# Kernel optimization log

Hardware: AMD Instinct MI355X
Metric: run time of the kernel (lower is better)

## Reference

```python
import jax, jax.numpy as jnp
import numpy as np

D_MODEL = 1024
DIM_K = 1024
DIM_V = 1024
N_HEADS = 16
B, SX, SY = 4, 1024, 1024
NORM_FACT = float(1.0 / np.sqrt(D_MODEL))  # note: 1/sqrt(d_model), not head dim


def setup_inputs() -> dict:
    key = jax.random.key(0)
    ks = jax.random.split(key, 10)
    s = 0.02
    return {
        "x": jax.random.normal(ks[0], (B, SX, D_MODEL), jnp.float32),
        "y": jax.random.normal(ks[1], (B, SY, D_MODEL), jnp.float32),
        "Wq": jax.random.normal(ks[2], (DIM_K, D_MODEL), jnp.float32) * s,
        "bq": jax.random.normal(ks[3], (DIM_K,), jnp.float32) * s,
        "Wk": jax.random.normal(ks[4], (DIM_K, D_MODEL), jnp.float32) * s,
        "bk": jax.random.normal(ks[5], (DIM_K,), jnp.float32) * s,
        "Wv": jax.random.normal(ks[6], (DIM_V, D_MODEL), jnp.float32) * s,
        "bv": jax.random.normal(ks[7], (DIM_V,), jnp.float32) * s,
        "Wo": jax.random.normal(ks[8], (D_MODEL, DIM_V), jnp.float32) * s,
        "bo": jax.random.normal(ks[9], (D_MODEL,), jnp.float32) * s,
        "requires_mask": 1,
    }


def reference(x, y, Wq, bq, Wk, bk, Wv, bv, Wo, bo, requires_mask):
    b, sx, _ = x.shape
    sy = y.shape[1]
    dk_h = DIM_K // N_HEADS
    dv_h = DIM_V // N_HEADS
    # torch: q(x).reshape(-1, B, S, dk_h) -> raw row-major reshape puts heads first
    Q = (x @ Wq.T + bq).reshape(N_HEADS, b, sx, dk_h)
    K = (y @ Wk.T + bk).reshape(N_HEADS, b, sy, dk_h)
    V = (y @ Wv.T + bv).reshape(N_HEADS, b, sy, dv_h)

    score = jnp.einsum('hbsd,hbtd->hbst', Q, K) * NORM_FACT  # [H,B,Sx,Sy]
    # branch 1: softmax over query axis (-2), then L1-normalize rows
    attn = jax.nn.softmax(score, axis=-2)
    l1 = jnp.maximum(jnp.sum(jnp.abs(attn), axis=-1, keepdims=True), 1e-12)
    attn = attn / l1
    # branch 2: mean-threshold mask then row softmax
    score1 = score
    if requires_mask:
        thre = jnp.mean(score, axis=-1, keepdims=True)
        score1 = jnp.where(score - thre > 0, score, -jnp.inf)
    attn1 = jax.nn.softmax(score1, axis=-1)

    # torch: matmul(...).reshape(B, Sx, -1) -> raw reshape of [H,B,Sx,dv_h]
    out = jnp.einsum('hbst,hbtd->hbsd', attn, V).reshape(b, sx, -1)
    out1 = jnp.einsum('hbst,hbtd->hbsd', attn1, V).reshape(b, sx, -1)
    out = 0.5 * (out + out1)
    return out @ Wo.T + bo
```

## Files before the change

kernel.cpp:

```cpp
#include <hip/hip_runtime.h>
#include <hip/hip_bf16.h>
#include <stdint.h>

typedef float f32x4 __attribute__((ext_vector_type(4)));
typedef short bf16x8 __attribute__((ext_vector_type(8)));
typedef _Float16 f16x8 __attribute__((ext_vector_type(8)));

#define DEV static __device__ __forceinline__

DEV float bf2f(short u) {
  union { float f; unsigned i; } v;
  v.i = ((unsigned)(unsigned short)u) << 16;
  return v.f;
}
DEV short f2bf(float f) {
  union { float f; unsigned i; } v;
  v.f = f;
  unsigned lsb = (v.i >> 16) & 1u;
  v.i += 0x7fffu + lsb;
  return (short)(v.i >> 16);
}
DEV short f2h(float f) {
  union { _Float16 h; short s; } u;
  u.h = (_Float16)f;
  return u.s;
}

DEV void glds16(const void* g, void* l) {
  __builtin_amdgcn_global_load_lds(
      (const __attribute__((address_space(1))) void*)g,
      (__attribute__((address_space(3))) void*)l, 16, 0, 0);
}

__global__ __launch_bounds__(256) void k_convert(
    const float* __restrict__ x, const float* __restrict__ y,
    const float* __restrict__ wq, const float* __restrict__ wk,
    const float* __restrict__ wv, const float* __restrict__ wo,
    short* __restrict__ x16, short* __restrict__ y16,
    short* __restrict__ wq16, short* __restrict__ wk16,
    short* __restrict__ wv16, short* __restrict__ wohi) {
  const float* src; short* dst; int n, half;
  switch (blockIdx.y) {
    case 0: src = x;  dst = x16;  n = 4194304; half = 1; break;
    case 1: src = y;  dst = y16;  n = 4194304; half = 1; break;
    case 2: src = wq; dst = wq16; n = 1048576; half = 1; break;
    case 3: src = wk; dst = wk16; n = 1048576; half = 1; break;
    case 4: src = wv; dst = wv16; n = 1048576; half = 1; break;
    default: src = wo; dst = wohi; n = 1048576; half = 0; break;
  }
  int i4 = blockIdx.x * 256 + threadIdx.x;
  if (i4 * 4 >= n) return;
  float4 v = ((const float4*)src)[i4];
  short4 h;
  float* pv = (float*)&v;
  short* ph = (short*)&h;
#pragma unroll
  for (int e = 0; e < 4; ++e) ph[e] = half ? f2h(pv[e]) : f2bf(pv[e]);
  ((short4*)dst)[i4] = h;
}

DEV void gemm_block_map(int wg, long& bRow, long& bCol) {
  int rlow = wg & 7, c = (wg >> 3) & 7, rhigh = wg >> 6;
  bRow = (long)(rhigh * 8 + rlow) * 128;
  bCol = (long)c * 128;
}

__global__ __launch_bounds__(512) void k_gemm_out(
    const short* __restrict__ A, const short* __restrict__ B,
    const float* __restrict__ bias, float* __restrict__ C, int M, int N, int K) {
  __shared__ __align__(16) short As[2][128 * 64];
  __shared__ __align__(16) short Bs[2][128 * 64];
  const int tid = threadIdx.x, lane = tid & 63;
  const int w = tid >> 6, wr = w >> 1, wc = w & 1;
  const int lo = lane & 15, hi4 = lane >> 4;
  long bRow, bCol;
  gemm_block_map(blockIdx.x, bRow, bCol);
  f32x4 acc[2][4] = {};
  const int nks = K >> 6;
  auto stage = [&](int buf, int ks) {
#pragma unroll
    for (int i = 0; i < 2; ++i) {
      int c = i * 512 + tid;
      int r = c >> 3;
      int wi = ((c & 7) * 16) ^ ((r & 7) << 4);
      glds16((const char*)A + (bRow + r) * (long)(K * 2) + ks * 128 + wi, (char*)As[buf] + c * 16);
      glds16((const char*)B + (bCol + r) * (long)(K * 2) + ks * 128 + wi, (char*)Bs[buf] + c * 16);
    }
  };
  stage(0, 0);
  __syncthreads();
  int p = 0;
  for (int ks = 0; ks < nks; ++ks) {
    if (ks + 1 < nks) stage(p ^ 1, ks + 1);
#pragma unroll
    for (int kk = 0; kk < 2; ++kk) {
      bf16x8 af[2], bfr[4];
#pragma unroll
      for (int m = 0; m < 2; ++m) {
        int r = wr * 32 + m * 16 + lo;
        af[m] = *(const bf16x8*)((const char*)As[p] + r * 128 + ((kk * 64 + hi4 * 16) ^ ((r & 7) << 4)));
      }
#pragma unroll
      for (int n = 0; n < 4; ++n) {
        int r = wc * 64 + n * 16 + lo;
        bfr[n] = *(const bf16x8*)((const char*)Bs[p] + r * 128 + ((kk * 64 + hi4 * 16) ^ ((r & 7) << 4)));
      }
#pragma unroll
      for (int m = 0; m < 2; ++m)
#pragma unroll
        for (int n = 0; n < 4; ++n)
          acc[m][n] = __builtin_amdgcn_mfma_f32_16x16x32_bf16(af[m], bfr[n], acc[m][n], 0, 0, 0);
    }
    __syncthreads();
    p ^= 1;
  }
#pragma unroll
  for (int n = 0; n < 4; ++n) {
    long col = bCol + wc * 64 + n * 16 + lo;
    float bv = bias[col];
#pragma unroll
    for (int m = 0; m < 2; ++m) {
      long row0 = bRow + wr * 32 + m * 16 + hi4 * 4;
#pragma unroll
      for (int j = 0; j < 4; ++j)
        C[(row0 + j) * N + col] = acc[m][n][j] + bv;
    }
  }
}

template <int OUT_MODE>
__global__ __launch_bounds__(512) void k_gemm_f16(
    const short* __restrict__ A, const short* __restrict__ B,
    const float* __restrict__ bias, short* __restrict__ C, int M, int N, int K) {
  __shared__ __align__(16) short As[2][128 * 64];
  __shared__ __align__(16) short Bs[2][128 * 64];
  const int tid = threadIdx.x, lane = tid & 63;
  const int w = tid >> 6, wr = w >> 1, wc = w & 1;
  const int lo = lane & 15, hi4 = lane >> 4;
  long bRow, bCol;
  gemm_block_map(blockIdx.x, bRow, bCol);
  f32x4 acc[2][4] = {};
  const int nks = K >> 6;
  auto stage = [&](int buf, int ks) {
#pragma unroll
    for (int i = 0; i < 2; ++i) {
      int c = i * 512 + tid;
      int r = c >> 3;
      int wi = ((c & 7) * 16) ^ ((r & 7) << 4);
      glds16((const char*)A + (bRow + r) * (long)(K * 2) + ks * 128 + wi, (char*)As[buf] + c * 16);
      glds16((const char*)B + (bCol + r) * (long)(K * 2) + ks * 128 + wi, (char*)Bs[buf] + c * 16);
    }
  };
  stage(0, 0);
  __syncthreads();
  int p = 0;
  for (int ks = 0; ks < nks; ++ks) {
    if (ks + 1 < nks) stage(p ^ 1, ks + 1);
#pragma unroll
    for (int kk = 0; kk < 2; ++kk) {
      f16x8 af[2], bfr[4];
#pragma unroll
      for (int m = 0; m < 2; ++m) {
        int r = wr * 32 + m * 16 + lo;
        af[m] = *(const f16x8*)((const char*)As[p] + r * 128 + ((kk * 64 + hi4 * 16) ^ ((r & 7) << 4)));
      }
#pragma unroll
      for (int n = 0; n < 4; ++n) {
        int r = wc * 64 + n * 16 + lo;
        bfr[n] = *(const f16x8*)((const char*)Bs[p] + r * 128 + ((kk * 64 + hi4 * 16) ^ ((r & 7) << 4)));
      }
#pragma unroll
      for (int m = 0; m < 2; ++m)
#pragma unroll
        for (int n = 0; n < 4; ++n)
          acc[m][n] = __builtin_amdgcn_mfma_f32_16x16x32_f16(af[m], bfr[n], acc[m][n], 0, 0, 0);
    }
    __syncthreads();
    p ^= 1;
  }
#pragma unroll
  for (int n = 0; n < 4; ++n) {
    long col = bCol + wc * 64 + n * 16 + lo;
    float bv = bias[col];
#pragma unroll
    for (int m = 0; m < 2; ++m)
#pragma unroll
      for (int j = 0; j < 4; ++j) {
        long row = bRow + wr * 32 + m * 16 + hi4 * 4 + j;
        float v = acc[m][n][j] + bv;
        C[row * N + col] = (OUT_MODE == 2) ? f2h(v) : f2bf(v);
      }
  }
}

__global__ __launch_bounds__(256) void k_transpose_scale(
    const short* __restrict__ Vb, const float* __restrict__ rL,
    short* __restrict__ Vt, short* __restrict__ rlbf) {
  __shared__ __align__(16) short T[64][264];
  int g = blockIdx.y, t0 = blockIdx.x * 256;
  int tid = threadIdx.x;
  const short* src = Vb + (long)g * 65536;
  const float* rlp = rL + g * 1024 + t0;
#pragma unroll
  for (int i = 0; i < 8; ++i) {
    int c = i * 256 + tid;
    int t = c >> 3, dc = (c & 7) * 8;
    bf16x8 v = *(const bf16x8*)(src + (long)(t0 + t) * 64 + dc);
    float rv = rlp[t];
#pragma unroll
    for (int e = 0; e < 8; ++e) T[dc + e][t] = f2bf(bf2f(v[e]) * rv);
  }
  rlbf[g * 1024 + t0 + tid] = f2bf(rlp[tid]);
  __syncthreads();
  short* dst = Vt + (long)g * 65536;
#pragma unroll
  for (int i = 0; i < 8; ++i) {
    int c = i * 256 + tid;
    int d = c >> 5, tc = (c & 31) * 8;
    bf16x8 v = *(const bf16x8*)(&T[d][tc]);
    *(bf16x8*)(dst + (long)d * 1024 + t0 + tc) = v;
  }
}

__global__ __launch_bounds__(256) void k_mu(
    const short* __restrict__ K16, const short* __restrict__ Q16,
    float* __restrict__ Thr) {
  __shared__ float tmp[32][64];
  __shared__ float ksum[64];
  const int g = blockIdx.x >> 2, q = blockIdx.x & 3;
  const int tid = threadIdx.x;
  const int d8 = tid & 7, tq = tid >> 3;
  const short* kp = K16 + (long)g * 65536;
  float acc[8] = {};
  for (int t = tq; t < 1024; t += 32) {
    f16x8 a = *(const f16x8*)(kp + t * 64 + d8 * 8);
#pragma unroll
    for (int e = 0; e < 8; ++e) acc[e] += (float)a[e];
  }
#pragma unroll
  for (int e = 0; e < 8; ++e) tmp[tq][d8 * 8 + e] = acc[e];
  __syncthreads();
  if (tid < 64) {
    float s = 0.f;
#pragma unroll
    for (int qq = 0; qq < 32; ++qq) s += tmp[qq][tid];
    ksum[tid] = s;
  }
  __syncthreads();
  const float c = 0.03125f / 1024.f;
  const int s = q * 256 + tid;
  const short* qp = Q16 + (long)g * 65536 + s * 64;
  float dot = 0.f;
#pragma unroll
  for (int d0 = 0; d0 < 64; d0 += 8) {
    f16x8 a = *(const f16x8*)(qp + d0);
#pragma unroll
    for (int e = 0; e < 8; ++e) dot += (float)a[e] * ksum[d0 + e];
  }
  Thr[g * 1024 + s] = dot * c;
}

__global__ __launch_bounds__(256) void k_passA(
    const short* __restrict__ Q16, const short* __restrict__ K16,
    float* __restrict__ rL) {
  __shared__ __align__(16) short Ks[64 * 64];
  __shared__ __align__(16) short Qs[2][64 * 64];
  const int wg = blockIdx.x;
  const int g = (wg & 7) | ((wg >> 7) << 3);
  const int tb = (wg >> 3) & 15;
  const int tid = threadIdx.x, lane = tid & 63;
  const int w = tid >> 6;
  const int lo = lane & 15, hi4 = lane >> 4;
  const long gbase = (long)g * 131072;
  const float CEXP = 0.045136860026163146f;

  auto stageQ = [&](int buf, int sb) {
#pragma unroll
    for (int i = 0; i < 2; ++i) {
      int c = i * 256 + tid;
      int r = c >> 3;
      int wi = ((c & 7) * 16) ^ ((r & 7) << 4);
      glds16((const char*)Q16 + gbase + (long)(sb * 64 + r) * 128 + wi, (char*)Qs[buf] + c * 16);
    }
  };
#pragma unroll
  for (int i = 0; i < 2; ++i) {
    int c = i * 256 + tid;
    int r = c >> 3;
    int wi = ((c & 7) * 16) ^ ((r & 7) << 4);
    glds16((const char*)K16 + gbase + (long)(tb * 64 + r) * 128 + wi, (char*)Ks + c * 16);
  }
  stageQ(0, 0);
  __syncthreads();
  f16x8 kf[2];
#pragma unroll
  for (int kk = 0; kk < 2; ++kk) {
    int r = w * 16 + lo;
    kf[kk] = *(const f16x8*)((const char*)Ks + r * 128 + ((kk * 64 + hi4 * 16) ^ ((r & 7) << 4)));
  }
  float Lacc[4] = {};
  int p = 0;
  for (int sb = 0; sb < 16; ++sb) {
    if (sb < 15) stageQ(p ^ 1, sb + 1);
    f32x4 s[4] = {};
#pragma unroll
    for (int kk = 0; kk < 2; ++kk) {
#pragma unroll
      for (int n = 0; n < 4; ++n) {
        int r = n * 16 + lo;
        f16x8 qf = *(const f16x8*)((const char*)Qs[p] + r * 128 +
                                   ((kk * 64 + hi4 * 16) ^ ((r & 7) << 4)));
        __builtin_amdgcn_s_setprio(1);
        s[n] = __builtin_amdgcn_mfma_f32_16x16x32_f16(kf[kk], qf, s[n], 0, 0, 0);
        __builtin_amdgcn_s_setprio(0);
      }
    }
#pragma unroll
    for (int n = 0; n < 4; ++n)
#pragma unroll
      for (int j = 0; j < 4; ++j)
        Lacc[j] += __builtin_amdgcn_exp2f(s[n][j] * CEXP);
    __syncthreads();
    p ^= 1;
  }
#pragma unroll
  for (int j = 0; j < 4; ++j) {
    float v = Lacc[j];
    v += __shfl_xor(v, 1);
    v += __shfl_xor(v, 2);
    v += __shfl_xor(v, 4);
    v += __shfl_xor(v, 8);
    if (lo == 0) rL[g * 1024 + tb * 64 + w * 16 + hi4 * 4 + j] = 1.0f / v;
  }
}

__global__ __launch_bounds__(256, 4) void k_passB(
    const short* __restrict__ Q16, const short* __restrict__ K16,
    const short* __restrict__ Vt, const short* __restrict__ rlbf,
    const float* __restrict__ Thr, short* __restrict__ Pre,
    const int* __restrict__ rmask) {
  __shared__ __align__(16) short Ks[2][64 * 64];
  __shared__ __align__(16) short Vs[2][64 * 64];
  __shared__ __align__(16) short Ps[64 * 64];
  const int wg = blockIdx.x;
  const int g = (wg & 7) | ((wg >> 7) << 3);
  const int rb = (wg >> 3) & 15;
  const int tid = threadIdx.x, lane = tid & 63;
  const int w = tid >> 6;
  const int lo = lane & 15, hi4 = lane >> 4;
  const long gbase = (long)g * 131072;
  const bool use_mask = (*rmask != 0);
  const int srow = w * 16 + lo;

  auto stage = [&](int buf, int tb2) {
#pragma unroll
    for (int i = 0; i < 2; ++i) {
      int c = i * 256 + tid;
      int r = c >> 3;
      int wi = ((c & 7) * 16) ^ ((r & 7) << 4);
      glds16((const char*)K16 + gbase + (long)(tb2 * 64 + r) * 128 + wi, (char*)Ks[buf] + c * 16);
      glds16((const char*)Vt + gbase + (long)r * 2048 + tb2 * 128 + wi, (char*)Vs[buf] + c * 16);
    }
  };

  f16x8 qf[2];
  {
    const char* qr = (const char*)Q16 + gbase + (long)(rb * 64 + srow) * 128;
#pragma unroll
    for (int kk = 0; kk < 2; ++kk)
      qf[kk] = *(const f16x8*)(qr + kk * 64 + hi4 * 16);
  }
  const float thre32 = use_mask ? Thr[g * 1024 + rb * 64 + srow] * 32.0f : -3.4e38f;
  const float CEXP = 0.045136860026163146f;
  f32x4 o1[4] = {}, o2[4] = {};
  f32x4 o1R = {}, o2Z = {};

  stage(0, 0);
  __syncthreads();
  int p = 0;
  for (int tb = 0; tb < 16; ++tb) {
    if (tb < 15) stage(p ^ 1, tb + 1);
    f32x4 s[4] = {};
#pragma unroll
    for (int kk = 0; kk < 2; ++kk) {
#pragma unroll
      for (int n = 0; n < 4; ++n) {
        int r = n * 16 + lo;
        f16x8 kf = *(const f16x8*)((const char*)Ks[p] + r * 128 +
                                   ((kk * 64 + hi4 * 16) ^ ((r & 7) << 4)));
        __builtin_amdgcn_s_setprio(1);
        s[n] = __builtin_amdgcn_mfma_f32_16x16x32_f16(kf, qf[kk], s[n], 0, 0, 0);
        __builtin_amdgcn_s_setprio(0);
      }
    }
    unsigned p2w0[4], p2w1[4];
#pragma unroll
    for (int n = 0; n < 4; ++n) {
      float ev[4], p2v[4];
#pragma unroll
      for (int j = 0; j < 4; ++j) {
        float sraw = s[n][j];
        float e = __builtin_amdgcn_exp2f(sraw * CEXP);
        ev[j] = e;
        p2v[j] = (sraw > thre32) ? e : 0.f;
      }
      unsigned u10, u11, u20, u21;
      asm("v_cvt_pk_bf16_f32 %0, %1, %2" : "=v"(u10) : "v"(ev[0]), "v"(ev[1]));
      asm("v_cvt_pk_bf16_f32 %0, %1, %2" : "=v"(u11) : "v"(ev[2]), "v"(ev[3]));
      asm("v_cvt_pk_bf16_f32 %0, %1, %2" : "=v"(u20) : "v"(p2v[0]), "v"(p2v[1]));
      asm("v_cvt_pk_bf16_f32 %0, %1, %2" : "=v"(u21) : "v"(p2v[2]), "v"(p2v[3]));
      p2w0[n] = u20;
      p2w1[n] = u21;
      int colb = n * 32 + hi4 * 8;
      int boff = srow * 128 + (colb ^ ((srow & 7) << 4));
      uint2 w1; w1.x = u10; w1.y = u11;
      *(uint2*)((char*)Ps + boff) = w1;
    }
    bf16x8 vbreg[2][4], rlfr[2];
#pragma unroll
    for (int kk = 0; kk < 2; ++kk) {
      int poff = srow * 128 + ((kk * 64 + hi4 * 16) ^ ((srow & 7) << 4));
      bf16x8 pa1 = *(const bf16x8*)((const char*)Ps + poff);
      rlfr[kk] = *(const bf16x8*)(rlbf + g * 1024 + tb * 64 + kk * 32 + hi4 * 8);
      __builtin_amdgcn_s_setprio(1);
      o1R = __builtin_amdgcn_mfma_f32_16x16x32_bf16(pa1, rlfr[kk], o1R, 0, 0, 0);
      __builtin_amdgcn_s_setprio(0);
#pragma unroll
      for (int n = 0; n < 4; ++n) {
        int d = n * 16 + lo;
        vbreg[kk][n] = *(const bf16x8*)((const char*)Vs[p] + d * 128 +
                                        ((kk * 64 + hi4 * 16) ^ ((d & 7) << 4)));
        __builtin_amdgcn_s_setprio(1);
        o1[n] = __builtin_amdgcn_mfma_f32_16x16x32_bf16(pa1, vbreg[kk][n], o1[n], 0, 0, 0);
        __builtin_amdgcn_s_setprio(0);
      }
    }
#pragma unroll
    for (int n = 0; n < 4; ++n) {
      int colb = n * 32 + hi4 * 8;
      int boff = srow * 128 + (colb ^ ((srow & 7) << 4));
      uint2 w2; w2.x = p2w0[n]; w2.y = p2w1[n];
      *(uint2*)((char*)Ps + boff) = w2;
    }
#pragma unroll
    for (int kk = 0; kk < 2; ++kk) {
      int poff = srow * 128 + ((kk * 64 + hi4 * 16) ^ ((srow & 7) << 4));
      bf16x8 pa2 = *(const bf16x8*)((const char*)Ps + poff);
      __builtin_amdgcn_s_setprio(1);
      o2Z = __builtin_amdgcn_mfma_f32_16x16x32_bf16(pa2, rlfr[kk], o2Z, 0, 0, 0);
#pragma unroll
      for (int n = 0; n < 4; ++n)
        o2[n] = __builtin_amdgcn_mfma_f32_16x16x32_bf16(pa2, vbreg[kk][n], o2[n], 0, 0, 0);
      __builtin_amdgcn_s_setprio(0);
    }
    __syncthreads();
    p ^= 1;
  }
#pragma unroll
  for (int j = 0; j < 4; ++j) {
    float rr = fmaxf(o1R[j], 1e-12f);
    float zz = fmaxf(o2Z[j], 1e-30f);
    float rinv = 0.5f / rr;
    float zinv = 0.5f / zz;
    int rl_ = w * 16 + hi4 * 4 + j;
#pragma unroll
    for (int n = 0; n < 4; ++n) {
      float val = o1[n][j] * rinv + o2[n][j] * zinv;
      Pre[(long)g * 65536 + (long)(rb * 64 + rl_) * 64 + n * 16 + lo] = f2bf(val);
    }
  }
}

extern "C" void kernel_launch(void* const* d_in, const int* in_sizes, int n_in,
                              void* d_out, int out_size, void* d_ws, size_t ws_size,
                              hipStream_t stream) {
  const float* x  = (const float*)d_in[0];
  const float* y  = (const float*)d_in[1];
  const float* Wq = (const float*)d_in[2];
  const float* bq = (const float*)d_in[3];
  const float* Wk = (const float*)d_in[4];
  const float* bk = (const float*)d_in[5];
  const float* Wv = (const float*)d_in[6];
  const float* bv = (const float*)d_in[7];
  const float* Wo = (const float*)d_in[8];
  const float* bo = (const float*)d_in[9];
  const int* rm   = (const int*)d_in[10];
  float* out = (float*)d_out;

  char* ws = (char*)d_ws;
  size_t off = 0;
  auto alloc = [&](size_t bytes) {
    char* p = ws + off;
    off += (bytes + 255) & ~(size_t)255;
    return p;
  };
  short* x16  = (short*)alloc(4194304 * 2);
  short* y16  = (short*)alloc(4194304 * 2);
  short* wq16 = (short*)alloc(1048576 * 2);
  short* wk16 = (short*)alloc(1048576 * 2);
  short* wv16 = (short*)alloc(1048576 * 2);
  short* wohi = (short*)alloc(1048576 * 2);
  short* Q16  = (short*)alloc(4194304 * 2);
  short* K16  = (short*)alloc(4194304 * 2);
  short* Vb   = (short*)alloc(4194304 * 2);
  short* VtB  = (short*)alloc(4194304 * 2);
  short* pre  = (short*)alloc(4194304 * 2);
  float* rLbuf = (float*)alloc(65536 * 4);
  short* rlbf  = (short*)alloc(65536 * 2);
  float* Thr   = (float*)alloc(65536 * 4);
  if (off > ws_size) return;

  k_convert<<<dim3(4096, 6), 256, 0, stream>>>(x, y, Wq, Wk, Wv, Wo,
                                               x16, y16, wq16, wk16, wv16, wohi);

  k_gemm_f16<2><<<256, 512, 0, stream>>>(x16, wq16, bq, Q16, 4096, 1024, 1024);
  k_gemm_f16<2><<<256, 512, 0, stream>>>(y16, wk16, bk, K16, 4096, 1024, 1024);
  k_gemm_f16<0><<<256, 512, 0, stream>>>(y16, wv16, bv, Vb, 4096, 1024, 1024);
  k_mu<<<256, 256, 0, stream>>>(K16, Q16, Thr);
  k_passA<<<1024, 256, 0, stream>>>(Q16, K16, rLbuf);
  k_transpose_scale<<<dim3(4, 64), 256, 0, stream>>>(Vb, rLbuf, VtB, rlbf);
  k_passB<<<1024, 256, 0, stream>>>(Q16, K16, VtB, rlbf, Thr, pre, rm);
  k_gemm_out<<<256, 512, 0, stream>>>(pre, wohi, bo, out, 4096, 1024, 1024);
}
```

Before: 161.2 us.

## Fuse V transpose-scale into passA and retile GEMMs to 128x64 blocks

Drops the separate transpose/scale kernel. Each passA block now loads its own 64-token V tile, scales it by the reciprocal column sums it just computed, transposes it through shared memory and writes Vt and the bf16 scales directly, which removes one launch and the fp32 rL round trip. All four GEMMs move from 512-thread 128x128 tiles to 256-thread 128x64 tiles with 512 blocks, giving more blocks per GPU and less shared memory per block at the cost of more A-tile reloads.

After: 156.0 us. 1.03x faster.

```diff
diff --git a/kernel.cpp b/kernel.cpp
--- a/kernel.cpp
+++ b/kernel.cpp
@@ -59,31 +59,37 @@
   ((short4*)dst)[i4] = h;
 }
 
-DEV void gemm_block_map(int wg, long& bRow, long& bCol) {
-  int rlow = wg & 7, c = (wg >> 3) & 7, rhigh = wg >> 6;
+DEV void gemm_block_map64(int wg, long& bRow, long& bCol) {
+  int rlow = wg & 7, c = (wg >> 3) & 15, rhigh = wg >> 7;
   bRow = (long)(rhigh * 8 + rlow) * 128;
-  bCol = (long)c * 128;
-}
-
-__global__ __launch_bounds__(512) void k_gemm_out(
+  bCol = (long)c * 64;
+}
+
+__global__ __launch_bounds__(256) void k_gemm_out(
     const short* __restrict__ A, const short* __restrict__ B,
     const float* __restrict__ bias, float* __restrict__ C, int M, int N, int K) {
   __shared__ __align__(16) short As[2][128 * 64];
-  __shared__ __align__(16) short Bs[2][128 * 64];
+  __shared__ __align__(16) short Bs[2][64 * 64];
   const int tid = threadIdx.x, lane = tid & 63;
-  const int w = tid >> 6, wr = w >> 1, wc = w & 1;
+  const int w = tid >> 6;
   const int lo = lane & 15, hi4 = lane >> 4;
   long bRow, bCol;
-  gemm_block_map(blockIdx.x, bRow, bCol);
+  gemm_block_map64(blockIdx.x, bRow, bCol);
   f32x4 acc[2][4] = {};
   const int nks = K >> 6;
   auto stage = [&](int buf, int ks) {
 #pragma unroll
-    for (int i = 0; i < 2; ++i) {
-      int c = i * 512 + tid;
+    for (int i = 0; i < 4; ++i) {
+      int c = i * 256 + tid;
       int r = c >> 3;
       int wi = ((c & 7) * 16) ^ ((r & 7) << 4);
       glds16((const char*)A + (bRow + r) * (long)(K * 2) + ks * 128 + wi, (char*)As[buf] + c * 16);
+    }
+#pragma unroll
+    for (int i = 0; i < 2; ++i) {
+      int c = i * 256 + tid;
+      int r = c >> 3;
+      int wi = ((c & 7) * 16) ^ ((r & 7) << 4);
       glds16((const char*)B + (bCol + r) * (long)(K * 2) + ks * 128 + wi, (char*)Bs[buf] + c * 16);
     }
   };
@@ -97,12 +103,12 @@
       bf16x8 af[2], bfr[4];
 #pragma unroll
       for (int m = 0; m < 2; ++m) {
-        int r = wr * 32 + m * 16 + lo;
+        int r = w * 32 + m * 16 + lo;
         af[m] = *(const bf16x8*)((const char*)As[p] + r * 128 + ((kk * 64 + hi4 * 16) ^ ((r & 7) << 4)));
       }
 #pragma unroll
       for (int n = 0; n < 4; ++n) {
-        int r = wc * 64 + n * 16 + lo;
+        int r = n * 16 + lo;
         bfr[n] = *(const bf16x8*)((const char*)Bs[p] + r * 128 + ((kk * 64 + hi4 * 16) ^ ((r & 7) << 4)));
       }
 #pragma unroll
@@ -116,11 +122,11 @@
   }
 #pragma unroll
   for (int n = 0; n < 4; ++n) {
-    long col = bCol + wc * 64 + n * 16 + lo;
+    long col = bCol + n * 16 + lo;
     float bv = bias[col];
 #pragma unroll
     for (int m = 0; m < 2; ++m) {
-      long row0 = bRow + wr * 32 + m * 16 + hi4 * 4;
+      long row0 = bRow + w * 32 + m * 16 + hi4 * 4;
 #pragma unroll
       for (int j = 0; j < 4; ++j)
         C[(row0 + j) * N + col] = acc[m][n][j] + bv;
@@ -129,25 +135,31 @@
 }
 
 template <int OUT_MODE>
-__global__ __launch_bounds__(512) void k_gemm_f16(
+__global__ __launch_bounds__(256) void k_gemm_f16(
     const short* __restrict__ A, const short* __restrict__ B,
     const float* __restrict__ bias, short* __restrict__ C, int M, int N, int K) {
   __shared__ __align__(16) short As[2][128 * 64];
-  __shared__ __align__(16) short Bs[2][128 * 64];
+  __shared__ __align__(16) short Bs[2][64 * 64];
   const int tid = threadIdx.x, lane = tid & 63;
-  const int w = tid >> 6, wr = w >> 1, wc = w & 1;
+  const int w = tid >> 6;
   const int lo = lane & 15, hi4 = lane >> 4;
   long bRow, bCol;
-  gemm_block_map(blockIdx.x, bRow, bCol);
+  gemm_block_map64(blockIdx.x, bRow, bCol);
   f32x4 acc[2][4] = {};
   const int nks = K >> 6;
   auto stage = [&](int buf, int ks) {
 #pragma unroll
-    for (int i = 0; i < 2; ++i) {
-      int c = i * 512 + tid;
+    for (int i = 0; i < 4; ++i) {
+      int c = i * 256 + tid;
       int r = c >> 3;
       int wi = ((c & 7) * 16) ^ ((r & 7) << 4);
       glds16((const char*)A + (bRow + r) * (long)(K * 2) + ks * 128 + wi, (char*)As[buf] + c * 16);
+    }
+#pragma unroll
+    for (int i = 0; i < 2; ++i) {
+      int c = i * 256 + tid;
+      int r = c >> 3;
+      int wi = ((c & 7) * 16) ^ ((r & 7) << 4);
       glds16((const char*)B + (bCol + r) * (long)(K * 2) + ks * 128 + wi, (char*)Bs[buf] + c * 16);
     }
   };
@@ -161,12 +173,12 @@
       f16x8 af[2], bfr[4];
 #pragma unroll
       for (int m = 0; m < 2; ++m) {
-        int r = wr * 32 + m * 16 + lo;
+        int r = w * 32 + m * 16 + lo;
         af[m] = *(const f16x8*)((const char*)As[p] + r * 128 + ((kk * 64 + hi4 * 16) ^ ((r & 7) << 4)));
       }
 #pragma unroll
       for (int n = 0; n < 4; ++n) {
-        int r = wc * 64 + n * 16 + lo;
+        int r = n * 16 + lo;
         bfr[n] = *(const f16x8*)((const char*)Bs[p] + r * 128 + ((kk * 64 + hi4 * 16) ^ ((r & 7) << 4)));
       }
 #pragma unroll
@@ -180,45 +192,16 @@
   }
 #pragma unroll
   for (int n = 0; n < 4; ++n) {
-    long col = bCol + wc * 64 + n * 16 + lo;
+    long col = bCol + n * 16 + lo;
     float bv = bias[col];
 #pragma unroll
     for (int m = 0; m < 2; ++m)
 #pragma unroll
       for (int j = 0; j < 4; ++j) {
-        long row = bRow + wr * 32 + m * 16 + hi4 * 4 + j;
+        long row = bRow + w * 32 + m * 16 + hi4 * 4 + j;
         float v = acc[m][n][j] + bv;
         C[row * N + col] = (OUT_MODE == 2) ? f2h(v) : f2bf(v);
       }
-  }
-}
-
-__global__ __launch_bounds__(256) void k_transpose_scale(
-    const short* __restrict__ Vb, const float* __restrict__ rL,
-    short* __restrict__ Vt, short* __restrict__ rlbf) {
-  __shared__ __align__(16) short T[64][264];
-  int g = blockIdx.y, t0 = blockIdx.x * 256;
-  int tid = threadIdx.x;
-  const short* src = Vb + (long)g * 65536;
-  const float* rlp = rL + g * 1024 + t0;
-#pragma unroll
-  for (int i = 0; i < 8; ++i) {
-    int c = i * 256 + tid;
-    int t = c >> 3, dc = (c & 7) * 8;
-    bf16x8 v = *(const bf16x8*)(src + (long)(t0 + t) * 64 + dc);
-    float rv = rlp[t];
-#pragma unroll
-    for (int e = 0; e < 8; ++e) T[dc + e][t] = f2bf(bf2f(v[e]) * rv);
-  }
-  rlbf[g * 1024 + t0 + tid] = f2bf(rlp[tid]);
-  __syncthreads();
-  short* dst = Vt + (long)g * 65536;
-#pragma unroll
-  for (int i = 0; i < 8; ++i) {
-    int c = i * 256 + tid;
-    int d = c >> 5, tc = (c & 31) * 8;
-    bf16x8 v = *(const bf16x8*)(&T[d][tc]);
-    *(bf16x8*)(dst + (long)d * 1024 + t0 + tc) = v;
   }
 }
 
@@ -260,11 +243,14 @@
   Thr[g * 1024 + s] = dot * c;
 }
 
-__global__ __launch_bounds__(256) void k_passA(
+__global__ __launch_bounds__(256) void k_passA_fuse(
     const short* __restrict__ Q16, const short* __restrict__ K16,
-    float* __restrict__ rL) {
+    const short* __restrict__ Vb, short* __restrict__ Vt,
+    short* __restrict__ rlbf) {
   __shared__ __align__(16) short Ks[64 * 64];
   __shared__ __align__(16) short Qs[2][64 * 64];
+  __shared__ __align__(16) short T[64][80];
+  __shared__ float rls[64];
   const int wg = blockIdx.x;
   const int g = (wg & 7) | ((wg >> 7) << 3);
   const int tb = (wg >> 3) & 15;
@@ -274,6 +260,14 @@
   const long gbase = (long)g * 131072;
   const float CEXP = 0.045136860026163146f;
 
+  const short* vsrc = Vb + (long)g * 65536 + (long)tb * 64 * 64;
+  bf16x8 vreg[2];
+#pragma unroll
+  for (int i = 0; i < 2; ++i) {
+    int c = i * 256 + tid;
+    vreg[i] = *(const bf16x8*)(vsrc + (c >> 3) * 64 + (c & 7) * 8);
+  }
+
   auto stageQ = [&](int buf, int sb) {
 #pragma unroll
     for (int i = 0; i < 2; ++i) {
@@ -330,7 +324,30 @@
     v += __shfl_xor(v, 2);
     v += __shfl_xor(v, 4);
     v += __shfl_xor(v, 8);
-    if (lo == 0) rL[g * 1024 + tb * 64 + w * 16 + hi4 * 4 + j] = 1.0f / v;
+    if (lo == 0) {
+      float rv = 1.0f / v;
+      int idx = w * 16 + hi4 * 4 + j;
+      rls[idx] = rv;
+      rlbf[g * 1024 + tb * 64 + idx] = f2bf(rv);
+    }
+  }
+  __syncthreads();
+#pragma unroll
+  for (int i = 0; i < 2; ++i) {
+    int c = i * 256 + tid;
+    int t = c >> 3, dc = (c & 7) * 8;
+    float rv = rls[t];
+#pragma unroll
+    for (int e = 0; e < 8; ++e) T[dc + e][t] = f2bf(bf2f(vreg[i][e]) * rv);
+  }
+  __syncthreads();
+  short* dst = Vt + (long)g * 65536 + tb * 64;
+#pragma unroll
+  for (int i = 0; i < 2; ++i) {
+    int c = i * 256 + tid;
+    int d = c >> 3, tc = (c & 7) * 8;
+    bf16x8 o = *(const bf16x8*)(&T[d][tc]);
+    *(bf16x8*)(dst + (long)d * 1024 + tc) = o;
   }
 }
 
@@ -505,20 +522,18 @@
   short* Vb   = (short*)alloc(4194304 * 2);
   short* VtB  = (short*)alloc(4194304 * 2);
   short* pre  = (short*)alloc(4194304 * 2);
-  float* rLbuf = (float*)alloc(65536 * 4);
-  short* rlbf  = (short*)alloc(65536 * 2);
-  float* Thr   = (float*)alloc(65536 * 4);
+  short* rlbf = (short*)alloc(65536 * 2);
+  float* Thr  = (float*)alloc(65536 * 4);
   if (off > ws_size) return;
 
   k_convert<<<dim3(4096, 6), 256, 0, stream>>>(x, y, Wq, Wk, Wv, Wo,
                                                x16, y16, wq16, wk16, wv16, wohi);
 
-  k_gemm_f16<2><<<256, 512, 0, stream>>>(x16, wq16, bq, Q16, 4096, 1024, 1024);
-  k_gemm_f16<2><<<256, 512, 0, stream>>>(y16, wk16, bk, K16, 4096, 1024, 1024);
-  k_gemm_f16<0><<<256, 512, 0, stream>>>(y16, wv16, bv, Vb, 4096, 1024, 1024);
+  k_gemm_f16<2><<<512, 256, 0, stream>>>(x16, wq16, bq, Q16, 4096, 1024, 1024);
+  k_gemm_f16<2><<<512, 256, 0, stream>>>(y16, wk16, bk, K16, 4096, 1024, 1024);
+  k_gemm_f16<0><<<512, 256, 0, stream>>>(y16, wv16, bv, Vb, 4096, 1024, 1024);
   k_mu<<<256, 256, 0, stream>>>(K16, Q16, Thr);
-  k_passA<<<1024, 256, 0, stream>>>(Q16, K16, rLbuf);
-  k_transpose_scale<<<dim3(4, 64), 256, 0, stream>>>(Vb, rLbuf, VtB, rlbf);
+  k_passA_fuse<<<1024, 256, 0, stream>>>(Q16, K16, Vb, VtB, rlbf);
   k_passB<<<1024, 256, 0, stream>>>(Q16, K16, VtB, rlbf, Thr, pre, rm);
-  k_gemm_out<<<256, 512, 0, stream>>>(pre, wohi, bo, out, 4096, 1024, 1024);
-}
+  k_gemm_out<<<512, 256, 0, stream>>>(pre, wohi, bo, out, 4096, 1024, 1024);
+}
```
